# Optimization experiments

Measured on AMD Instinct MI355X. Metric: run time of the kernel, lower is better.

Reference implementation:

```python
import jax, jax.numpy as jnp
import numpy as np

B, T, D, H = 2, 2048, 2048, 16
DH = D // H

def setup_inputs() -> dict:
    key = jax.random.key(0)
    k1, k2, k3 = jax.random.split(key, 3)
    x = jax.random.normal(k1, (B, T, D), dtype=jnp.float32)
    w_qkv = jax.random.normal(k2, (D, 3 * D), dtype=jnp.float32) * (1.0 / np.sqrt(D))
    w_o = jax.random.normal(k3, (D, D), dtype=jnp.float32) * (1.0 / np.sqrt(D))
    return {"x": x, "w_qkv": w_qkv, "w_o": w_o}

def reference(x, w_qkv, w_o):
    b, t, d = x.shape
    qkv = (x @ w_qkv).reshape(b, t, 3, H, DH)
    q, k, v = qkv[:, :, 0], qkv[:, :, 1], qkv[:, :, 2]  # [b,t,h,dh]
    scale = 1.0 / np.sqrt(DH).astype(np.float32)
    # scores: [b,h,t,t]
    scores = jnp.einsum('bqhd,bkhd->bhqk', q, k) * scale
    causal = jnp.tril(jnp.ones((t, t), dtype=bool))
    scores = jnp.where(causal[None, None], scores, -jnp.inf)
    attn = jax.nn.softmax(scores, axis=-1)
    out = jnp.einsum('bhqk,bkhd->bqhd', attn, v).reshape(b, t, d)
    return out @ w_o
```

## Files before the change

### kernel.cpp

```cpp
#include <hip/hip_runtime.h>
#include <hip/hip_bf16.h>

#define B_   2
#define T_   2048
#define D_   2048
#define H_   16
#define DH_  128
#define TD3_ 6144

typedef __attribute__((ext_vector_type(8))) short   short8;
typedef __attribute__((ext_vector_type(8))) unsigned short ushort8v;
typedef __attribute__((ext_vector_type(4))) float   f32x4;
typedef __attribute__((ext_vector_type(4))) float   f4v;
typedef __attribute__((ext_vector_type(4))) unsigned short u16x4;

static __device__ __forceinline__ unsigned short f2bf(float f) {
  unsigned int u = __builtin_bit_cast(unsigned int, f);
  u += 0x7FFFu + ((u >> 16) & 1u);
  return (unsigned short)(u >> 16);
}
static __device__ __forceinline__ float bf2f(unsigned short u) {
  return __builtin_bit_cast(float, (unsigned int)u << 16);
}

static __device__ __forceinline__ void gload_lds16(const unsigned short* g, unsigned short* l) {
  __builtin_amdgcn_global_load_lds((const __attribute__((address_space(1))) void*)g,
                                   (__attribute__((address_space(3))) void*)l, 16, 0, 0);
}

__global__ __launch_bounds__(256) void convert_f32_bf16(const float* __restrict__ X,
                                                        unsigned short* __restrict__ Y, int n4) {
  for (int i = blockIdx.x * blockDim.x + threadIdx.x; i < n4; i += gridDim.x * blockDim.x) {
    f4v v = ((const f4v*)X)[i];
    u16x4 o;
    o[0] = f2bf(v[0]); o[1] = f2bf(v[1]); o[2] = f2bf(v[2]); o[3] = f2bf(v[3]);
    ((u16x4*)Y)[i] = o;
  }
}

__global__ __launch_bounds__(256) void transpose_f32_bf16(const float* __restrict__ W,
                                                          unsigned short* __restrict__ WT,
                                                          int K, int N) {
  __shared__ float tile[32][33];
  int n0 = blockIdx.x * 32, k0 = blockIdx.y * 32;
  int tx = threadIdx.x & 31, ty = threadIdx.x >> 5;
#pragma unroll
  for (int r = 0; r < 4; r++)
    tile[ty + 8 * r][tx] = W[(size_t)(k0 + ty + 8 * r) * N + n0 + tx];
  __syncthreads();
#pragma unroll
  for (int r = 0; r < 4; r++)
    WT[(size_t)(n0 + ty + 8 * r) * K + k0 + tx] = f2bf(tile[tx][ty + 8 * r]);
}

__global__ __launch_bounds__(256) void vtr_kernel(const unsigned short* __restrict__ qkv,
                                                  unsigned short* __restrict__ vtg) {
  __shared__ unsigned short tile[64][68];
  const int t0 = blockIdx.x * 64;
  const int h = blockIdx.y >> 1, dh0 = (blockIdx.y & 1) * 64;
  const int b = blockIdx.z;
  const int tid = threadIdx.x;
  const unsigned short* src = qkv + (size_t)b * T_ * TD3_ + 2 * D_ + h * DH_ + dh0;
  {
    const int r = tid >> 3, cc = (tid & 7) * 8;
#pragma unroll
    for (int k = 0; k < 2; k++) {
      ushort8v v = *(const ushort8v*)(src + (size_t)(t0 + k * 32 + r) * TD3_ + cc);
      *(ushort8v*)&tile[k * 32 + r][cc] = v;
    }
  }
  __syncthreads();
  unsigned short* dst = vtg + ((size_t)(b * H_ + h) * DH_ + dh0) * T_ + t0;
  {
    const int d = tid >> 3, tc = (tid & 7) * 8;
#pragma unroll
    for (int k = 0; k < 2; k++) {
      ushort8v v;
#pragma unroll
      for (int j = 0; j < 8; j++) v[j] = tile[tc + j][k * 32 + d];
      *(ushort8v*)(dst + (size_t)(k * 32 + d) * T_ + tc) = v;
    }
  }
}

__global__ __launch_bounds__(512, 1) void gemm_qkv192(const unsigned short* __restrict__ A,
                                                      const unsigned short* __restrict__ BT,
                                                      unsigned short* __restrict__ C,
                                                      int M, int N, int K) {
  __shared__ unsigned short lA[2][2][128 * 64];
  __shared__ unsigned short lB[2][192 * 64];

  const int tid = threadIdx.x;
  const int bid = (int)blockIdx.x;
  const int npx = 4;
  const int xcd = bid & 7, idx = bid >> 3;
  const int n0 = (xcd * npx + (idx & 3)) * 192;
  const int m0 = (idx >> 2) * 256;
  const int l = tid & 63, lr = l & 15, lg = l >> 4;
  const int wid = tid >> 6, wm = wid >> 2, wn = wid & 3;
  const int nk = K >> 6;

  f32x4 acc[8][3] = {};

  auto stageA = [&](int buf, int h, int kt) {
#pragma unroll
    for (int q = 0; q < 2; q++) {
      const int n = q * 512 + tid;
      const int row = n >> 3, ch = n & 7;
      gload_lds16(A + (size_t)(m0 + h * 128 + row) * K + kt * 64 + ((ch ^ (row & 7)) << 3),
                  &lA[buf][h][n * 8]);
    }
  };
  auto stageBt = [&](int buf, int third, int kt) {
    const int r = tid >> 3, ch = tid & 7;
    gload_lds16(BT + (size_t)(n0 + third * 64 + r) * K + kt * 64 + ((ch ^ (r & 7)) << 3),
                &lB[buf][third * 4096 + tid * 8]);
  };

  stageA(0, 0, 0); stageA(0, 1, 0);
  stageBt(0, 0, 0); stageBt(0, 1, 0); stageBt(0, 2, 0);
  if (nk > 1) {
    stageBt(1, 0, 1); stageBt(1, 1, 1); stageBt(1, 2, 1);
    asm volatile("s_waitcnt vmcnt(3)" ::: "memory");
  } else {
    asm volatile("s_waitcnt vmcnt(0)" ::: "memory");
  }
  __builtin_amdgcn_s_barrier();

  short8 a[4][2], b[3][2];
  for (int kt = 0; kt < nk; kt++) {
    const int buf = kt & 1;

#pragma unroll
    for (int mi = 0; mi < 4; mi++)
#pragma unroll
      for (int kk = 0; kk < 2; kk++) {
        const int row = mi * 16 + lr;
        a[mi][kk] = *(const short8*)&lA[buf][wm][row * 64 + (((kk * 4 + lg) ^ (lr & 7)) << 3)];
      }
#pragma unroll
    for (int ni = 0; ni < 3; ni++)
#pragma unroll
      for (int kk = 0; kk < 2; kk++) {
        const int row = wn * 48 + ni * 16 + lr;
        b[ni][kk] = *(const short8*)&lB[buf][row * 64 + (((kk * 4 + lg) ^ (lr & 7)) << 3)];
      }
    if (kt + 1 < nk) stageA(buf ^ 1, 0, kt + 1);
    __builtin_amdgcn_s_barrier();
    __builtin_amdgcn_s_setprio(1);
#pragma unroll
    for (int mi = 0; mi < 4; mi++)
#pragma unroll
      for (int ni = 0; ni < 2; ni++)
#pragma unroll
        for (int kk = 0; kk < 2; kk++)
          acc[mi][ni] = __builtin_amdgcn_mfma_f32_16x16x32_bf16(a[mi][kk], b[ni][kk], acc[mi][ni], 0, 0, 0);
    __builtin_amdgcn_s_setprio(0);
    __builtin_amdgcn_s_barrier();

    if (kt + 1 < nk) stageA(buf ^ 1, 1, kt + 1);
    if (kt + 2 < nk) stageBt(buf, 0, kt + 2);
    __builtin_amdgcn_s_barrier();
    __builtin_amdgcn_s_setprio(1);
#pragma unroll
    for (int mi = 0; mi < 4; mi++)
#pragma unroll
      for (int kk = 0; kk < 2; kk++)
        acc[mi][2] = __builtin_amdgcn_mfma_f32_16x16x32_bf16(a[mi][kk], b[2][kk], acc[mi][2], 0, 0, 0);
    __builtin_amdgcn_s_setprio(0);
    __builtin_amdgcn_s_barrier();

#pragma unroll
    for (int mi = 0; mi < 4; mi++)
#pragma unroll
      for (int kk = 0; kk < 2; kk++) {
        const int row = (4 + mi) * 16 + lr;
        a[mi][kk] = *(const short8*)&lA[buf][wm][row * 64 + (((kk * 4 + lg) ^ (lr & 7)) << 3)];
      }
    if (kt + 2 < nk) stageBt(buf, 1, kt + 2);
    __builtin_amdgcn_s_barrier();
    __builtin_amdgcn_s_setprio(1);
#pragma unroll
    for (int mi = 0; mi < 4; mi++)
#pragma unroll
      for (int ni = 0; ni < 2; ni++)
#pragma unroll
        for (int kk = 0; kk < 2; kk++)
          acc[4 + mi][ni] = __builtin_amdgcn_mfma_f32_16x16x32_bf16(a[mi][kk], b[ni][kk], acc[4 + mi][ni], 0, 0, 0);
    __builtin_amdgcn_s_setprio(0);
    __builtin_amdgcn_s_barrier();

    if (kt + 2 < nk) stageBt(buf, 2, kt + 2);
    __builtin_amdgcn_s_barrier();
    __builtin_amdgcn_s_setprio(1);
#pragma unroll
    for (int mi = 0; mi < 4; mi++)
#pragma unroll
      for (int kk = 0; kk < 2; kk++)
        acc[4 + mi][2] = __builtin_amdgcn_mfma_f32_16x16x32_bf16(a[mi][kk], b[2][kk], acc[4 + mi][2], 0, 0, 0);
    __builtin_amdgcn_s_setprio(0);
    if (kt + 2 < nk) asm volatile("s_waitcnt vmcnt(3)" ::: "memory");
    else             asm volatile("s_waitcnt vmcnt(0)" ::: "memory");
    __builtin_amdgcn_s_barrier();
  }

#pragma unroll
  for (int mi = 0; mi < 8; mi++)
#pragma unroll
    for (int ni = 0; ni < 3; ni++)
#pragma unroll
      for (int i = 0; i < 4; i++) {
        const int row = m0 + wm * 128 + mi * 16 + lg * 4 + i;
        const int col = n0 + wn * 48 + ni * 16 + lr;
        C[(size_t)row * N + col] = f2bf(acc[mi][ni][i]);
      }
}

__global__ __launch_bounds__(512, 1) void gemm_op8(const unsigned short* __restrict__ A,
                                                   const unsigned short* __restrict__ BT,
                                                   float* __restrict__ C,
                                                   int M, int N, int K) {
  __shared__ unsigned short lA[2][128 * 64];
  __shared__ unsigned short lB[2][2][128 * 64];

  const int tid = threadIdx.x;
  const int bid = (int)blockIdx.x;
  const int xcd = bid & 7, idx = bid >> 3;
  const int n0 = xcd * 256, m0 = idx * 128;
  const int l = tid & 63, lr = l & 15, lg = l >> 4;
  const int wid = tid >> 6, wm = wid >> 2, wn = wid & 3;
  const int bh = wn >> 1, br0 = (wn & 1) * 64;
  const int nk = K >> 6;

  f32x4 acc[4][4] = {};

  auto stageA = [&](int buf, int kt) {
#pragma unroll
    for (int q = 0; q < 2; q++) {
      const int n = q * 512 + tid;
      const int row = n >> 3, ch = n & 7;
      gload_lds16(A + (size_t)(m0 + row) * K + kt * 64 + ((ch ^ (row & 7)) << 3),
                  &lA[buf][n * 8]);
    }
  };
  auto stageB = [&](int buf, int h, int kt) {
#pragma unroll
    for (int q = 0; q < 2; q++) {
      const int n = q * 512 + tid;
      const int row = n >> 3, ch = n & 7;
      gload_lds16(BT + (size_t)(n0 + h * 128 + row) * K + kt * 64 + ((ch ^ (row & 7)) << 3),
                  &lB[buf][h][n * 8]);
    }
  };

  stageB(0, 0, 0); stageB(0, 1, 0); stageA(0, 0);
  if (nk > 1) {
    stageB(1, 0, 1); stageB(1, 1, 1); stageA(1, 1);
    asm volatile("s_waitcnt vmcnt(6)" ::: "memory");
  } else {
    asm volatile("s_waitcnt vmcnt(0)" ::: "memory");
  }
  __builtin_amdgcn_s_barrier();

  short8 a[2][2], b0[2][2], b1[2][2];
  for (int kt = 0; kt < nk; kt++) {
    const int buf = kt & 1;

#pragma unroll
    for (int mi = 0; mi < 2; mi++)
#pragma unroll
      for (int kk = 0; kk < 2; kk++) {
        const int row = wm * 64 + mi * 16 + lr;
        a[mi][kk] = *(const short8*)&lA[buf][row * 64 + (((kk * 4 + lg) ^ (lr & 7)) << 3)];
      }
#pragma unroll
    for (int ni = 0; ni < 2; ni++)
#pragma unroll
      for (int kk = 0; kk < 2; kk++) {
        const int row = br0 + ni * 16 + lr;
        b0[ni][kk] = *(const short8*)&lB[buf][bh][row * 64 + (((kk * 4 + lg) ^ (lr & 7)) << 3)];
      }
    __builtin_amdgcn_s_barrier();
    __builtin_amdgcn_s_setprio(1);
#pragma unroll
    for (int mi = 0; mi < 2; mi++)
#pragma unroll
      for (int ni = 0; ni < 2; ni++)
#pragma unroll
        for (int kk = 0; kk < 2; kk++)
          acc[mi][ni] = __builtin_amdgcn_mfma_f32_16x16x32_bf16(a[mi][kk], b0[ni][kk], acc[mi][ni], 0, 0, 0);
    __builtin_amdgcn_s_setprio(0);
    __builtin_amdgcn_s_barrier();

#pragma unroll
    for (int ni = 0; ni < 2; ni++)
#pragma unroll
      for (int kk = 0; kk < 2; kk++) {
        const int row = br0 + (2 + ni) * 16 + lr;
        b1[ni][kk] = *(const short8*)&lB[buf][bh][row * 64 + (((kk * 4 + lg) ^ (lr & 7)) << 3)];
      }
    __builtin_amdgcn_s_barrier();
    __builtin_amdgcn_s_setprio(1);
#pragma unroll
    for (int mi = 0; mi < 2; mi++)
#pragma unroll
      for (int ni = 0; ni < 2; ni++)
#pragma unroll
        for (int kk = 0; kk < 2; kk++)
          acc[mi][2 + ni] = __builtin_amdgcn_mfma_f32_16x16x32_bf16(a[mi][kk], b1[ni][kk], acc[mi][2 + ni], 0, 0, 0);
    __builtin_amdgcn_s_setprio(0);
    __builtin_amdgcn_s_barrier();

#pragma unroll
    for (int mi = 0; mi < 2; mi++)
#pragma unroll
      for (int kk = 0; kk < 2; kk++) {
        const int row = wm * 64 + (2 + mi) * 16 + lr;
        a[mi][kk] = *(const short8*)&lA[buf][row * 64 + (((kk * 4 + lg) ^ (lr & 7)) << 3)];
      }
    if (kt + 2 < nk) stageB(buf, 0, kt + 2);
    __builtin_amdgcn_s_barrier();
    __builtin_amdgcn_s_setprio(1);
#pragma unroll
    for (int mi = 0; mi < 2; mi++)
#pragma unroll
      for (int ni = 0; ni < 2; ni++)
#pragma unroll
        for (int kk = 0; kk < 2; kk++)
          acc[2 + mi][2 + ni] = __builtin_amdgcn_mfma_f32_16x16x32_bf16(a[mi][kk], b1[ni][kk], acc[2 + mi][2 + ni], 0, 0, 0);
    __builtin_amdgcn_s_setprio(0);
    __builtin_amdgcn_s_barrier();

    if (kt + 2 < nk) { stageB(buf, 1, kt + 2); stageA(buf, kt + 2); }
    __builtin_amdgcn_s_barrier();
    __builtin_amdgcn_s_setprio(1);
#pragma unroll
    for (int mi = 0; mi < 2; mi++)
#pragma unroll
      for (int ni = 0; ni < 2; ni++)
#pragma unroll
        for (int kk = 0; kk < 2; kk++)
          acc[2 + mi][ni] = __builtin_amdgcn_mfma_f32_16x16x32_bf16(a[mi][kk], b0[ni][kk], acc[2 + mi][ni], 0, 0, 0);
    __builtin_amdgcn_s_setprio(0);
    if (kt + 2 < nk) asm volatile("s_waitcnt vmcnt(6)" ::: "memory");
    else             asm volatile("s_waitcnt vmcnt(0)" ::: "memory");
    __builtin_amdgcn_s_barrier();
  }

#pragma unroll
  for (int mi = 0; mi < 4; mi++)
#pragma unroll
    for (int ni = 0; ni < 4; ni++)
#pragma unroll
      for (int i = 0; i < 4; i++) {
        const int row = m0 + wm * 64 + mi * 16 + lg * 4 + i;
        const int col = n0 + wn * 64 + ni * 16 + lr;
        C[(size_t)row * N + col] = acc[mi][ni][i];
      }
}

__global__ __launch_bounds__(256, 2) void attn_fa(const unsigned short* __restrict__ qkv,
                                                  const unsigned short* __restrict__ vtg,
                                                  unsigned short* __restrict__ out) {
  const int x = blockIdx.x, h = blockIdx.y, b = blockIdx.z;
  const int qtl = b ? x : (T_ / 128 - 1 - x);
  const int q0 = qtl * 128;
  const int tid = threadIdx.x, w = tid >> 6, l = tid & 63, lr = l & 15, lg = l >> 4;

  const unsigned short* Qb = qkv + (size_t)b * T_ * TD3_ + h * DH_;
  const unsigned short* Kb = Qb + D_;
  const unsigned short* Vt = vtg + ((size_t)b * H_ + h) * DH_ * T_;

  __shared__ unsigned short klds[2][64 * 128];
  __shared__ unsigned short vt[2][128 * 64];
  __shared__ unsigned short plds[4][32 * 64];

  const float scale = 0.08838834764831845f;

  short8 qf[2][4];
#pragma unroll
  for (int mi = 0; mi < 2; mi++) {
    const unsigned short* qrow = Qb + (size_t)(q0 + w * 32 + mi * 16 + lr) * TD3_;
#pragma unroll
    for (int ks = 0; ks < 4; ks++) {
      ushort8v qv = *(const ushort8v*)(qrow + ks * 32 + lg * 8);
      short8 qs;
#pragma unroll
      for (int j = 0; j < 8; j++) qs[j] = (short)f2bf(bf2f(qv[j]) * scale);
      qf[mi][ks] = qs;
    }
  }

  f32x4 oacc[2][8] = {};
  float mrun[2][4], lsum[2][4];
#pragma unroll
  for (int mi = 0; mi < 2; mi++)
#pragma unroll
    for (int i = 0; i < 4; i++) { mrun[mi][i] = -__builtin_inff(); lsum[mi][i] = 0.f; }

  auto STAGE = [&](int buf, int kv0) {
#pragma unroll
    for (int it = 0; it < 4; it++) {
      const int n = it * 256 + tid;
      { const int kv = n >> 4, ch = n & 15;
        gload_lds16(Kb + (size_t)(kv0 + kv) * TD3_ + ((ch ^ (kv & 7)) << 3),
                    &klds[buf][n * 8]); }
      { const int dh = n >> 3, ch = n & 7;
        gload_lds16(Vt + (size_t)dh * T_ + kv0 + ((ch ^ (dh & 7)) << 3),
                    &vt[buf][n * 8]); }
    }
  };

  const int nt = 2 * qtl + 2;
  STAGE(0, 0);
  __syncthreads();

  for (int t = 0; t < nt; t++) {
    const int buf = t & 1;
    if (t + 1 < nt) STAGE(buf ^ 1, (t + 1) * 64);

    const int kv0 = t * 64;
    const bool active = (kv0 <= q0 + w * 32 + 31);
    if (active) {
      f32x4 s[2][4] = {};
      __builtin_amdgcn_s_setprio(1);
#pragma unroll
      for (int nf = 0; nf < 4; nf++) {
        const int kv = nf * 16 + lr;
#pragma unroll
        for (int ks = 0; ks < 4; ks++) {
          short8 kf = *(const short8*)&klds[buf][kv * 128 + (((ks * 4 + lg) ^ (lr & 7)) << 3)];
#pragma unroll
          for (int mi = 0; mi < 2; mi++)
            s[mi][nf] = __builtin_amdgcn_mfma_f32_16x16x32_bf16(qf[mi][ks], kf, s[mi][nf], 0, 0, 0);
        }
      }
      __builtin_amdgcn_s_setprio(0);

      const bool needmask = (kv0 + 63 > q0 + w * 32);
      float pmax[2][4];
#pragma unroll
      for (int mi = 0; mi < 2; mi++)
#pragma unroll
        for (int i = 0; i < 4; i++) pmax[mi][i] = -__builtin_inff();
#pragma unroll
      for (int mi = 0; mi < 2; mi++)
#pragma unroll
        for (int nf = 0; nf < 4; nf++)
#pragma unroll
          for (int i = 0; i < 4; i++) {
            float xv = s[mi][nf][i];
            if (needmask) {
              const int qr = w * 32 + mi * 16 + lg * 4 + i;
              const int kc = nf * 16 + lr;
              if (kv0 + kc > q0 + qr) xv = -__builtin_inff();
            }
            s[mi][nf][i] = xv;
            pmax[mi][i] = fmaxf(pmax[mi][i], xv);
          }
#pragma unroll
      for (int m = 1; m < 16; m <<= 1)
#pragma unroll
        for (int mi = 0; mi < 2; mi++)
#pragma unroll
          for (int i = 0; i < 4; i++) pmax[mi][i] = fmaxf(pmax[mi][i], __shfl_xor(pmax[mi][i], m));

      float alpha[2][4], rsum[2][4];
#pragma unroll
      for (int mi = 0; mi < 2; mi++)
#pragma unroll
        for (int i = 0; i < 4; i++) {
          const float mn = fmaxf(mrun[mi][i], pmax[mi][i]);
          alpha[mi][i] = __expf(mrun[mi][i] - mn);
          mrun[mi][i] = mn;
          rsum[mi][i] = 0.f;
        }
#pragma unroll
      for (int mi = 0; mi < 2; mi++)
#pragma unroll
        for (int nf = 0; nf < 4; nf++)
#pragma unroll
          for (int i = 0; i < 4; i++) {
            const float p = __expf(s[mi][nf][i] - mrun[mi][i]);
            rsum[mi][i] += p;
            const int prow = mi * 16 + lg * 4 + i;
            plds[w][prow * 64 + ((nf * 16 + lr) ^ ((prow & 7) << 3))] = f2bf(p);
          }
#pragma unroll
      for (int m = 1; m < 16; m <<= 1)
#pragma unroll
        for (int mi = 0; mi < 2; mi++)
#pragma unroll
          for (int i = 0; i < 4; i++) rsum[mi][i] += __shfl_xor(rsum[mi][i], m);
#pragma unroll
      for (int mi = 0; mi < 2; mi++)
#pragma unroll
        for (int i = 0; i < 4; i++) lsum[mi][i] = lsum[mi][i] * alpha[mi][i] + rsum[mi][i];
#pragma unroll
      for (int mi = 0; mi < 2; mi++)
#pragma unroll
        for (int nf = 0; nf < 8; nf++)
#pragma unroll
          for (int i = 0; i < 4; i++) oacc[mi][nf][i] *= alpha[mi][i];

      __builtin_amdgcn_s_setprio(1);
#pragma unroll
      for (int kk = 0; kk < 2; kk++) {
        short8 pa[2];
#pragma unroll
        for (int mi = 0; mi < 2; mi++) {
          const int prow = mi * 16 + lr;
          pa[mi] = *(const short8*)&plds[w][prow * 64 + (((kk * 32 + lg * 8)) ^ ((prow & 7) << 3))];
        }
#pragma unroll
        for (int nf = 0; nf < 8; nf++) {
          const short8 vb = *(const short8*)&vt[buf][(nf * 16 + lr) * 64 + (((kk * 4 + lg) ^ (lr & 7)) << 3)];
#pragma unroll
          for (int mi = 0; mi < 2; mi++)
            oacc[mi][nf] = __builtin_amdgcn_mfma_f32_16x16x32_bf16(pa[mi], vb, oacc[mi][nf], 0, 0, 0);
        }
      }
      __builtin_amdgcn_s_setprio(0);
    }
    __syncthreads();
  }

  float rinv[2][4];
#pragma unroll
  for (int mi = 0; mi < 2; mi++)
#pragma unroll
    for (int i = 0; i < 4; i++) rinv[mi][i] = 1.f / lsum[mi][i];
#pragma unroll
  for (int mi = 0; mi < 2; mi++) {
    unsigned short* orow = out + ((size_t)b * T_ + q0 + w * 32 + mi * 16 + lg * 4) * D_ + h * DH_;
#pragma unroll
    for (int nf = 0; nf < 8; nf++)
#pragma unroll
      for (int i = 0; i < 4; i++)
        orow[(size_t)i * D_ + nf * 16 + lr] = f2bf(oacc[mi][nf][i] * rinv[mi][i]);
  }
}

extern "C" void kernel_launch(void* const* d_in, const int* in_sizes, int n_in,
                              void* d_out, int out_size, void* d_ws, size_t ws_size,
                              hipStream_t stream) {
  const float* x    = (const float*)d_in[0];
  const float* wqkv = (const float*)d_in[1];
  const float* wo   = (const float*)d_in[2];
  float* out = (float*)d_out;

  char* ws = (char*)d_ws;
  unsigned short* xb    = (unsigned short*)(ws);
  unsigned short* wqkvt = (unsigned short*)(ws + 16777216);
  unsigned short* vtg   = (unsigned short*)(ws + 16777216);
  unsigned short* wot   = (unsigned short*)(ws + 41943040);
  unsigned short* qkv   = (unsigned short*)(ws + 50331648);
  unsigned short* attn  = xb;

  convert_f32_bf16<<<2048, 256, 0, stream>>>(x, xb, B_ * T_ * D_ / 4);
  transpose_f32_bf16<<<dim3(TD3_ / 32, D_ / 32), 256, 0, stream>>>(wqkv, wqkvt, D_, TD3_);
  transpose_f32_bf16<<<dim3(D_ / 32, D_ / 32), 256, 0, stream>>>(wo, wot, D_, D_);

  gemm_qkv192<<<dim3(512), 512, 0, stream>>>(xb, wqkvt, qkv, B_ * T_, TD3_, D_);
  vtr_kernel<<<dim3(T_ / 64, H_ * 2, B_), 256, 0, stream>>>(qkv, vtg);
  attn_fa<<<dim3(T_ / 128, H_, B_), 256, 0, stream>>>(qkv, vtg, attn);
  gemm_op8<<<dim3(256), 512, 0, stream>>>(attn, wot, out, B_ * T_, D_, D_);
}
```

Before: 302.4 us.

## Restructure QKV GEMM loop into two-phase schedule with register double-buffered fragments

Rewrites the QKV projection GEMM main loop. Each k-tile is now two phases. The whole next tile (A and B) is staged into the alternate LDS buffer at the start. LDS fragment reads for the next tile go into a second register set (bX/bY) while the current tile's MFMAs finish. This cuts the number of barriers per k-tile from about eight to two and overlaps LDS reads with MFMA work. The costs are a shallower global prefetch (one tile ahead with a full vmcnt(0) wait instead of two tiles for B), more fragment registers, and an unrolled-by-two loop that assumes an even number of k-tiles.

```diff
diff --git a/kernel.cpp b/kernel.cpp
--- a/kernel.cpp
+++ b/kernel.cpp
@@ -101,6 +101,7 @@
   const int nk = K >> 6;
 
   f32x4 acc[8][3] = {};
+  short8 aQ0[4][2], aQ1[4][2], bX[3][2], bY[3][2];
 
   auto stageA = [&](int buf, int h, int kt) {
 #pragma unroll
@@ -117,91 +118,87 @@
                 &lB[buf][third * 4096 + tid * 8]);
   };
 
-  stageA(0, 0, 0); stageA(0, 1, 0);
-  stageBt(0, 0, 0); stageBt(0, 1, 0); stageBt(0, 2, 0);
-  if (nk > 1) {
-    stageBt(1, 0, 1); stageBt(1, 1, 1); stageBt(1, 2, 1);
-    asm volatile("s_waitcnt vmcnt(3)" ::: "memory");
-  } else {
-    asm volatile("s_waitcnt vmcnt(0)" ::: "memory");
-  }
+#define QKV_STAGE_ALL(BUF, TT)                                                  \
+  { stageA(BUF, 0, TT); stageA(BUF, 1, TT);                                     \
+    stageBt(BUF, 0, TT); stageBt(BUF, 1, TT); stageBt(BUF, 2, TT); }
+
+#define QKV_READ_A(DST, BUF, QUAD)                                              \
+  _Pragma("unroll")                                                             \
+  for (int mi = 0; mi < 4; mi++)                                                \
+    _Pragma("unroll")                                                           \
+    for (int kk = 0; kk < 2; kk++) {                                            \
+      const int row = ((QUAD) * 4 + mi) * 16 + lr;                              \
+      DST[mi][kk] = *(const short8*)&lA[BUF][wm][row * 64 +                     \
+                      (((kk * 4 + lg) ^ (lr & 7)) << 3)];                       \
+    }
+
+#define QKV_READ_B(DST, BUF)                                                    \
+  _Pragma("unroll")                                                             \
+  for (int ni = 0; ni < 3; ni++)                                                \
+    _Pragma("unroll")                                                           \
+    for (int kk = 0; kk < 2; kk++) {                                            \
+      const int row = wn * 48 + ni * 16 + lr;                                   \
+      DST[ni][kk] = *(const short8*)&lB[BUF][row * 64 +                         \
+                      (((kk * 4 + lg) ^ (lr & 7)) << 3)];                       \
+    }
+
+#define QKV_PHASE_A(BUF, BCUR, TT)                                              \
+  {                                                                             \
+    if ((TT) + 1 < nk) QKV_STAGE_ALL(1 - (BUF), (TT) + 1);                      \
+    QKV_READ_A(aQ1, BUF, 1)                                                     \
+    __builtin_amdgcn_s_setprio(1);                                              \
+    _Pragma("unroll")                                                           \
+    for (int mi = 0; mi < 4; mi++)                                              \
+      _Pragma("unroll")                                                         \
+      for (int ni = 0; ni < 3; ni++)                                            \
+        _Pragma("unroll")                                                       \
+        for (int kk = 0; kk < 2; kk++)                                          \
+          acc[mi][ni] = __builtin_amdgcn_mfma_f32_16x16x32_bf16(                \
+              aQ0[mi][kk], BCUR[ni][kk], acc[mi][ni], 0, 0, 0);                 \
+    __builtin_amdgcn_s_setprio(0);                                              \
+    __builtin_amdgcn_s_barrier();                                               \
+  }
+
+#define QKV_PHASE_B(BUF, BCUR, BNXT, TT)                                        \
+  {                                                                             \
+    __builtin_amdgcn_s_setprio(1);                                              \
+    _Pragma("unroll")                                                           \
+    for (int mi = 0; mi < 4; mi++)                                              \
+      _Pragma("unroll")                                                         \
+      for (int ni = 0; ni < 2; ni++)                                            \
+        _Pragma("unroll")                                                       \
+        for (int kk = 0; kk < 2; kk++)                                          \
+          acc[4 + mi][ni] = __builtin_amdgcn_mfma_f32_16x16x32_bf16(            \
+              aQ1[mi][kk], BCUR[ni][kk], acc[4 + mi][ni], 0, 0, 0);             \
+    __builtin_amdgcn_s_setprio(0);                                              \
+    asm volatile("s_waitcnt vmcnt(0)" ::: "memory");                            \
+    __builtin_amdgcn_s_barrier();                                               \
+    if ((TT) + 1 < nk) {                                                        \
+      QKV_READ_A(aQ0, 1 - (BUF), 0)                                             \
+      QKV_READ_B(BNXT, 1 - (BUF))                                               \
+    }                                                                           \
+    __builtin_amdgcn_s_setprio(1);                                              \
+    _Pragma("unroll")                                                           \
+    for (int mi = 0; mi < 4; mi++)                                              \
+      _Pragma("unroll")                                                         \
+      for (int kk = 0; kk < 2; kk++)                                            \
+        acc[4 + mi][2] = __builtin_amdgcn_mfma_f32_16x16x32_bf16(               \
+            aQ1[mi][kk], BCUR[2][kk], acc[4 + mi][2], 0, 0, 0);                 \
+    __builtin_amdgcn_s_setprio(0);                                              \
+    __builtin_amdgcn_s_barrier();                                               \
+  }
+
+  QKV_STAGE_ALL(0, 0)
+  asm volatile("s_waitcnt vmcnt(0)" ::: "memory");
   __builtin_amdgcn_s_barrier();
-
-  short8 a[4][2], b[3][2];
-  for (int kt = 0; kt < nk; kt++) {
-    const int buf = kt & 1;
-
-#pragma unroll
-    for (int mi = 0; mi < 4; mi++)
-#pragma unroll
-      for (int kk = 0; kk < 2; kk++) {
-        const int row = mi * 16 + lr;
-        a[mi][kk] = *(const short8*)&lA[buf][wm][row * 64 + (((kk * 4 + lg) ^ (lr & 7)) << 3)];
-      }
-#pragma unroll
-    for (int ni = 0; ni < 3; ni++)
-#pragma unroll
-      for (int kk = 0; kk < 2; kk++) {
-        const int row = wn * 48 + ni * 16 + lr;
-        b[ni][kk] = *(const short8*)&lB[buf][row * 64 + (((kk * 4 + lg) ^ (lr & 7)) << 3)];
-      }
-    if (kt + 1 < nk) stageA(buf ^ 1, 0, kt + 1);
-    __builtin_amdgcn_s_barrier();
-    __builtin_amdgcn_s_setprio(1);
-#pragma unroll
-    for (int mi = 0; mi < 4; mi++)
-#pragma unroll
-      for (int ni = 0; ni < 2; ni++)
-#pragma unroll
-        for (int kk = 0; kk < 2; kk++)
-          acc[mi][ni] = __builtin_amdgcn_mfma_f32_16x16x32_bf16(a[mi][kk], b[ni][kk], acc[mi][ni], 0, 0, 0);
-    __builtin_amdgcn_s_setprio(0);
-    __builtin_amdgcn_s_barrier();
-
-    if (kt + 1 < nk) stageA(buf ^ 1, 1, kt + 1);
-    if (kt + 2 < nk) stageBt(buf, 0, kt + 2);
-    __builtin_amdgcn_s_barrier();
-    __builtin_amdgcn_s_setprio(1);
-#pragma unroll
-    for (int mi = 0; mi < 4; mi++)
-#pragma unroll
-      for (int kk = 0; kk < 2; kk++)
-        acc[mi][2] = __builtin_amdgcn_mfma_f32_16x16x32_bf16(a[mi][kk], b[2][kk], acc[mi][2], 0, 0, 0);
-    __builtin_amdgcn_s_setprio(0);
-    __builtin_amdgcn_s_barrier();
-
-#pragma unroll
-    for (int mi = 0; mi < 4; mi++)
-#pragma unroll
-      for (int kk = 0; kk < 2; kk++) {
-        const int row = (4 + mi) * 16 + lr;
-        a[mi][kk] = *(const short8*)&lA[buf][wm][row * 64 + (((kk * 4 + lg) ^ (lr & 7)) << 3)];
-      }
-    if (kt + 2 < nk) stageBt(buf, 1, kt + 2);
-    __builtin_amdgcn_s_barrier();
-    __builtin_amdgcn_s_setprio(1);
-#pragma unroll
-    for (int mi = 0; mi < 4; mi++)
-#pragma unroll
-      for (int ni = 0; ni < 2; ni++)
-#pragma unroll
-        for (int kk = 0; kk < 2; kk++)
-          acc[4 + mi][ni] = __builtin_amdgcn_mfma_f32_16x16x32_bf16(a[mi][kk], b[ni][kk], acc[4 + mi][ni], 0, 0, 0);
-    __builtin_amdgcn_s_setprio(0);
-    __builtin_amdgcn_s_barrier();
-
-    if (kt + 2 < nk) stageBt(buf, 2, kt + 2);
-    __builtin_amdgcn_s_barrier();
-    __builtin_amdgcn_s_setprio(1);
-#pragma unroll
-    for (int mi = 0; mi < 4; mi++)
-#pragma unroll
-      for (int kk = 0; kk < 2; kk++)
-        acc[4 + mi][2] = __builtin_amdgcn_mfma_f32_16x16x32_bf16(a[mi][kk], b[2][kk], acc[4 + mi][2], 0, 0, 0);
-    __builtin_amdgcn_s_setprio(0);
-    if (kt + 2 < nk) asm volatile("s_waitcnt vmcnt(3)" ::: "memory");
-    else             asm volatile("s_waitcnt vmcnt(0)" ::: "memory");
-    __builtin_amdgcn_s_barrier();
+  QKV_READ_A(aQ0, 0, 0)
+  QKV_READ_B(bX, 0)
+
+  for (int kt = 0; kt < nk; kt += 2) {
+    QKV_PHASE_A(0, bX, kt)
+    QKV_PHASE_B(0, bX, bY, kt)
+    QKV_PHASE_A(1, bY, kt + 1)
+    QKV_PHASE_B(1, bY, bX, kt + 1)
   }
 
 #pragma unroll
@@ -214,6 +211,11 @@
         const int col = n0 + wn * 48 + ni * 16 + lr;
         C[(size_t)row * N + col] = f2bf(acc[mi][ni][i]);
       }
+#undef QKV_PHASE_B
+#undef QKV_PHASE_A
+#undef QKV_READ_B
+#undef QKV_READ_A
+#undef QKV_STAGE_ALL
 }
 
 __global__ __launch_bounds__(512, 1) void gemm_op8(const unsigned short* __restrict__ A,
```

After: 284.8 us. 1.06x faster.
